# Kernel tuning notes

Hardware: AMD Instinct MI355X
Metric: run time of the kernel (lower is better)

## Reference

```python
import jax, jax.numpy as jnp
import numpy as np

B, S, D, H = 2, 2048, 1024, 16
HD = D // H
NEG = -10000000000.0

def setup_inputs() -> dict:
    key = jax.random.key(0)
    ks = jax.random.split(key, 9)
    s = 1.0 / np.sqrt(D)
    return {
        "x": jax.random.normal(ks[0], (B, S, D), dtype=jnp.float32),
        "Wq": jax.random.uniform(ks[1], (D, D), jnp.float32, -s, s),
        "bq": jax.random.uniform(ks[2], (D,), jnp.float32, -s, s),
        "Wk": jax.random.uniform(ks[3], (D, D), jnp.float32, -s, s),
        "bk": jax.random.uniform(ks[4], (D,), jnp.float32, -s, s),
        "Wv": jax.random.uniform(ks[5], (D, D), jnp.float32, -s, s),
        "bv": jax.random.uniform(ks[6], (D,), jnp.float32, -s, s),
        "Wo": jax.random.uniform(ks[7], (D, D), jnp.float32, -s, s),
        "bo": jax.random.uniform(ks[8], (D,), jnp.float32, -s, s),
    }

def reference(x, Wq, bq, Wk, bk, Wv, bv, Wo, bo):
    b, s, _ = x.shape
    def split_heads(t):
        return t.reshape(b, s, H, HD).transpose(0, 2, 1, 3)  # [b,h,s,hd]
    Q = split_heads(x @ Wq + bq)
    K = split_heads(x @ Wk + bk)
    V = split_heads(x @ Wv + bv)
    scores = jnp.einsum('bhqd,bhkd->bhqk', Q, K) / jnp.sqrt(jnp.float32(HD))
    causal = jnp.tril(jnp.ones((s, s), dtype=bool))
    scores = jnp.where(causal[None, None], scores, NEG)
    attn = jax.nn.softmax(scores, axis=-1)
    ctx = jnp.einsum('bhqk,bhkd->bhqd', attn, V)
    ctx = ctx.transpose(0, 2, 1, 3).reshape(b, s, D)
    return ctx @ Wo + bo
```

## Files before the change

### kernel.cpp

```cpp
#include <hip/hip_runtime.h>
#include <hip/hip_bf16.h>

#define BB 2
#define SS 2048
#define DD 1024
#define HH 16
#define HD 64
#define MM (BB*SS)

typedef __attribute__((ext_vector_type(8))) short bf16x8;
typedef __attribute__((ext_vector_type(4))) float f32x4;
typedef __attribute__((ext_vector_type(16))) float f32x16;

#define QSCALE 0.18033688f

static __device__ __forceinline__ unsigned short f2bf(float f) {
    unsigned int u = __builtin_bit_cast(unsigned int, f);
    u += 0x7fffu + ((u >> 16) & 1u);
    return (unsigned short)(u >> 16);
}

static __device__ __forceinline__ void gload16(const unsigned short* g, unsigned short* l) {
    __builtin_amdgcn_global_load_lds(
        (const __attribute__((address_space(1))) unsigned int*)g,
        (__attribute__((address_space(3))) unsigned int*)l, 16, 0, 0);
}

__global__ __launch_bounds__(256) void prep_kernel(const float* __restrict__ x,
                                                   const float* __restrict__ W0,
                                                   const float* __restrict__ W1,
                                                   const float* __restrict__ W2,
                                                   const float* __restrict__ W3,
                                                   unsigned short* __restrict__ xb,
                                                   unsigned short* __restrict__ Wt)
{
    const int t = threadIdx.x;
    const int bid = blockIdx.x;
    if (bid < 2048) {
        const size_t i = ((size_t)bid * 256 + t) * 8;
        float4 a = *(const float4*)(x + i);
        float4 b = *(const float4*)(x + i + 4);
        union { unsigned short u[8]; bf16x8 v; } pk;
        pk.u[0] = f2bf(a.x); pk.u[1] = f2bf(a.y); pk.u[2] = f2bf(a.z); pk.u[3] = f2bf(a.w);
        pk.u[4] = f2bf(b.x); pk.u[5] = f2bf(b.y); pk.u[6] = f2bf(b.z); pk.u[7] = f2bf(b.w);
        *(bf16x8*)(xb + i) = pk.v;
        return;
    }
    __shared__ unsigned short Ts[64][72];
    const int wsel = (bid - 2048) >> 8;
    const int rem  = (bid - 2048) & 255;
    const float* W = wsel == 0 ? W0 : wsel == 1 ? W1 : wsel == 2 ? W2 : W3;
    unsigned short* out = Wt + (size_t)wsel * DD * DD;
    const int n0 = (rem & 15) * 64, k0 = (rem >> 4) * 64;
#pragma unroll
    for (int i = 0; i < 4; ++i) {
        const int r = (t >> 4) + i * 16;
        const int c = (t & 15) * 4;
        float4 v = *(const float4*)(W + (size_t)(k0 + r) * DD + n0 + c);
        Ts[c + 0][r] = f2bf(v.x); Ts[c + 1][r] = f2bf(v.y);
        Ts[c + 2][r] = f2bf(v.z); Ts[c + 3][r] = f2bf(v.w);
    }
    __syncthreads();
#pragma unroll
    for (int j = 0; j < 2; ++j) {
        const int ch = j * 256 + t;
        const int rn = ch >> 3, ck = (ch & 7) * 8;
        bf16x8 v = *(const bf16x8*)&Ts[rn][ck];
        *(bf16x8*)(out + (size_t)(n0 + rn) * DD + k0 + ck) = v;
    }
}

__global__ __launch_bounds__(256) void gemm_mfma(const unsigned short* __restrict__ A,
                                                 const unsigned short* __restrict__ Bt,
                                                 const float* __restrict__ bias0,
                                                 const float* __restrict__ bias1,
                                                 const float* __restrict__ bias2,
                                                 unsigned short* __restrict__ Qb,
                                                 unsigned short* __restrict__ Kb,
                                                 unsigned short* __restrict__ Vb,
                                                 float* __restrict__ outf,
                                                 int mode)
{
    __shared__ unsigned short As[2][128 * 64];
    __shared__ unsigned short Bs[2][128 * 64];

    const int t = threadIdx.x;
    const int w = t >> 6, l = t & 63;
    const int lane16 = l & 15, quad = l >> 4;
    const int m0 = blockIdx.x * 128, n0 = blockIdx.y * 128;
    const int wm = (w & 1) * 64, wn = (w >> 1) * 64;

    f32x4 acc[4][4] = {};

    int srow[4], skcg[4];
#pragma unroll
    for (int j = 0; j < 4; ++j) {
        const int c = t + j * 256;
        srow[j] = c >> 3;
        skcg[j] = (c & 7) ^ (srow[j] & 7);
    }

#pragma unroll
    for (int j = 0; j < 4; ++j) {
        const int c = t + j * 256;
        gload16(A  + (size_t)(m0 + srow[j]) * DD + skcg[j] * 8, &As[0][c * 8]);
        gload16(Bt + (size_t)(n0 + srow[j]) * DD + skcg[j] * 8, &Bs[0][c * 8]);
    }
    __syncthreads();

#pragma unroll 2
    for (int kt = 0; kt < 16; ++kt) {
        const int cur = kt & 1;
        if (kt + 1 < 16) {
            const int k1 = (kt + 1) * 64;
#pragma unroll
            for (int j = 0; j < 4; ++j) {
                const int c = t + j * 256;
                gload16(A  + (size_t)(m0 + srow[j]) * DD + k1 + skcg[j] * 8, &As[cur ^ 1][c * 8]);
                gload16(Bt + (size_t)(n0 + srow[j]) * DD + k1 + skcg[j] * 8, &Bs[cur ^ 1][c * 8]);
            }
        }
#pragma unroll
        for (int h = 0; h < 2; ++h) {
            bf16x8 af[4], bfr[4];
#pragma unroll
            for (int mt = 0; mt < 4; ++mt) {
                const int row = wm + mt * 16 + lane16;
                af[mt] = *(const bf16x8*)&As[cur][(row * 8 + ((h * 4 + quad) ^ (row & 7))) * 8];
            }
#pragma unroll
            for (int nt = 0; nt < 4; ++nt) {
                const int row = wn + nt * 16 + lane16;
                bfr[nt] = *(const bf16x8*)&Bs[cur][(row * 8 + ((h * 4 + quad) ^ (row & 7))) * 8];
            }
#pragma unroll
            for (int mt = 0; mt < 4; ++mt)
#pragma unroll
                for (int nt = 0; nt < 4; ++nt)
                    acc[mt][nt] = __builtin_amdgcn_mfma_f32_16x16x32_bf16(af[mt], bfr[nt], acc[mt][nt], 0, 0, 0);
        }
        __syncthreads();
    }

    if (mode == 0) {
        const int which = n0 >> 10;
        const float* bias = which == 0 ? bias0 : which == 1 ? bias1 : bias2;
#pragma unroll
        for (int nt = 0; nt < 4; ++nt) {
            const int gcol = n0 + wn + nt * 16 + lane16;
            const int cd = gcol & 1023;
            const float bv = bias[cd];
            const int h_ = cd >> 6, d = cd & 63;
            if (which == 2) {
#pragma unroll
                for (int mt = 0; mt < 4; ++mt) {
                    const int row0 = m0 + wm + mt * 16 + quad * 4;
                    const int b_ = row0 >> 11, s0 = row0 & 2047;
                    union { unsigned short u[4]; uint2 v; } pk;
#pragma unroll
                    for (int r = 0; r < 4; ++r) pk.u[r] = f2bf(acc[mt][nt][r] + bv);
                    *(uint2*)(Vb + ((size_t)(b_ * HH + h_) * HD + d) * SS + s0) = pk.v;
                }
            } else {
                unsigned short* dst3 = which == 0 ? Qb : Kb;
                const float sc_ = which == 0 ? QSCALE : 1.0f;
#pragma unroll
                for (int mt = 0; mt < 4; ++mt)
#pragma unroll
                    for (int r = 0; r < 4; ++r) {
                        const int row = m0 + wm + mt * 16 + quad * 4 + r;
                        const int b_ = row >> 11, s_ = row & 2047;
                        dst3[(((size_t)(b_ * HH + h_) * SS + s_) * HD) + d] =
                            f2bf((acc[mt][nt][r] + bv) * sc_);
                    }
            }
        }
    } else {
#pragma unroll
        for (int nt = 0; nt < 4; ++nt) {
            const int gcol = n0 + wn + nt * 16 + lane16;
            const float bv = bias0[gcol];
#pragma unroll
            for (int mt = 0; mt < 4; ++mt)
#pragma unroll
                for (int r = 0; r < 4; ++r) {
                    const int row = m0 + wm + mt * 16 + quad * 4 + r;
                    outf[(size_t)row * DD + gcol] = acc[mt][nt][r] + bv;
                }
        }
    }
}

__global__ __launch_bounds__(512) void attn_mfma(const unsigned short* __restrict__ Q,
                                                 const unsigned short* __restrict__ K,
                                                 const unsigned short* __restrict__ V,
                                                 unsigned short* __restrict__ ctx)
{
    __shared__ unsigned short Ks[4][4096];
    __shared__ unsigned short Vs[4][4096];

    const int t = threadIdx.x;
    const int w = t >> 6, l = t & 63;
    const int l31 = l & 31, hi = l >> 5;
    const int qg = w & 3, par = w >> 2;
    const int bid = blockIdx.x;
    const int halfg = bid >> 8, idx = bid & 255;
    const int qb_ = idx >> 5;
    const int qblk = halfg ? qb_ : 15 - qb_;
    const int hb = idx & 31;
    const int h = hb & 15, b = hb >> 4;
    const int q0 = qblk * 128;
    const size_t bh = (size_t)(b * HH + h) * SS;
    const unsigned short* Vg = V + (size_t)(b * HH + h) * HD * SS;

    const int wq0 = q0 + qg * 32;
    bf16x8 qf[4];
#pragma unroll
    for (int dt = 0; dt < 4; ++dt)
        qf[dt] = *(const bf16x8*)(Q + (bh + wq0 + l31) * HD + dt * 16 + hi * 8);

    f32x16 ot[2] = {};
    float lp = 0.f;

    const int ntiles = 2 * qblk + 2;
    const int sr = t >> 3;
    const int sg = (t & 7) ^ (sr & 7);

    {
        gload16(K  + (bh + sr) * HD + sg * 8,            &Ks[0][t * 8]);
        gload16(K  + (bh + 64 + sr) * HD + sg * 8,       &Ks[1][t * 8]);
        gload16(Vg + (size_t)sr * SS + sg * 8,           &Vs[0][t * 8]);
        gload16(Vg + (size_t)sr * SS + 64 + sg * 8,      &Vs[1][t * 8]);
    }
    __syncthreads();

    const int nsup = ntiles >> 1;
    for (int st = 0; st < nsup; ++st) {
        if (2 * st + 2 < ntiles) {
            const int ka = (2 * st + 2) * 64, kb = ka + 64;
            const int ba = (2 * st + 2) & 3, bb2 = (2 * st + 3) & 3;
            gload16(K  + (bh + ka + sr) * HD + sg * 8,       &Ks[ba][t * 8]);
            gload16(K  + (bh + kb + sr) * HD + sg * 8,       &Ks[bb2][t * 8]);
            gload16(Vg + (size_t)sr * SS + ka + sg * 8,      &Vs[ba][t * 8]);
            gload16(Vg + (size_t)sr * SS + kb + sg * 8,      &Vs[bb2][t * 8]);
        }

        const int mt = 2 * st + par;
        const int k0 = mt * 64;
        if (k0 <= wq0 + 31) {
            const unsigned short* Kt = Ks[mt & 3];
            const unsigned short* Vt = Vs[mt & 3];

            f32x16 s[2] = {};
#pragma unroll
            for (int dt = 0; dt < 4; ++dt) {
#pragma unroll
                for (int kh = 0; kh < 2; ++kh) {
                    const int row = kh * 32 + l31;
                    bf16x8 kf = *(const bf16x8*)&Kt[(row * 8 + ((dt * 2 + hi) ^ (row & 7))) * 8];
                    s[kh] = __builtin_amdgcn_mfma_f32_32x32x16_bf16(kf, qf[dt], s[kh], 0, 0, 0);
                }
            }

            if (k0 + 63 > wq0) {
                const int q = wq0 + l31;
#pragma unroll
                for (int kh = 0; kh < 2; ++kh)
#pragma unroll
                    for (int r = 0; r < 16; ++r) {
                        const int k = k0 + kh * 32 + (r & 3) + 8 * (r >> 2) + 4 * hi;
                        if (k > q) s[kh][r] = -1e30f;
                    }
            }

#pragma unroll
            for (int kh = 0; kh < 2; ++kh) {
#pragma unroll
                for (int r = 0; r < 16; ++r) s[kh][r] = __builtin_amdgcn_exp2f(s[kh][r]);
                const float t0 = (s[kh][0] + s[kh][1]) + (s[kh][2] + s[kh][3]);
                const float t1 = (s[kh][4] + s[kh][5]) + (s[kh][6] + s[kh][7]);
                const float t2 = (s[kh][8] + s[kh][9]) + (s[kh][10] + s[kh][11]);
                const float t3 = (s[kh][12] + s[kh][13]) + (s[kh][14] + s[kh][15]);
                lp += (t0 + t1) + (t2 + t3);
            }

#pragma unroll
            for (int kh = 0; kh < 2; ++kh) {
#pragma unroll
                for (int c = 0; c < 2; ++c) {
                    const int rb = c * 8;
                    unsigned int w0, w1, w2, w3;
                    asm("v_cvt_pk_bf16_f32 %0, %1, %2" : "=v"(w0) : "v"(s[kh][rb + 0]), "v"(s[kh][rb + 1]));
                    asm("v_cvt_pk_bf16_f32 %0, %1, %2" : "=v"(w2) : "v"(s[kh][rb + 4]), "v"(s[kh][rb + 5]));
                    asm("v_cvt_pk_bf16_f32 %0, %1, %2" : "=v"(w1) : "v"(s[kh][rb + 2]), "v"(s[kh][rb + 3]));
                    asm("v_cvt_pk_bf16_f32 %0, %1, %2" : "=v"(w3) : "v"(s[kh][rb + 6]), "v"(s[kh][rb + 7]));
                    asm("v_permlane32_swap_b32 %0, %1" : "+v"(w0), "+v"(w2));
                    asm("v_permlane32_swap_b32 %0, %1" : "+v"(w1), "+v"(w3));
                    union { unsigned int u[4]; bf16x8 v; } pa;
                    pa.u[0] = w0; pa.u[1] = w1; pa.u[2] = w2; pa.u[3] = w3;
                    const int chunk = kh * 4 + c * 2 + hi;
                    const int rlo = l31, rhi2 = 32 + l31;
                    bf16x8 v0 = *(const bf16x8*)&Vt[(rlo * 8 + (chunk ^ (rlo & 7))) * 8];
                    bf16x8 v1 = *(const bf16x8*)&Vt[(rhi2 * 8 + (chunk ^ (rhi2 & 7))) * 8];
                    ot[0] = __builtin_amdgcn_mfma_f32_32x32x16_bf16(v0, pa.v, ot[0], 0, 0, 0);
                    ot[1] = __builtin_amdgcn_mfma_f32_32x32x16_bf16(v1, pa.v, ot[1], 0, 0, 0);
                }
            }
        }
        __syncthreads();
    }

    float* Osh = (float*)&Ks[0][0];
    float* Lsh = (float*)&Vs[0][0];
    if (par == 1) {
        float* o = Osh + qg * 2048;
#pragma unroll
        for (int a2 = 0; a2 < 2; ++a2)
#pragma unroll
            for (int r = 0; r < 16; ++r) o[(a2 * 16 + r) * 64 + l] = ot[a2][r];
        Lsh[qg * 64 + l] = lp;
    }
    __syncthreads();
    if (par == 0) {
        float* o = Osh + qg * 2048;
#pragma unroll
        for (int a2 = 0; a2 < 2; ++a2)
#pragma unroll
            for (int r = 0; r < 16; ++r) ot[a2][r] += o[(a2 * 16 + r) * 64 + l];
        lp += Lsh[qg * 64 + l];

        lp += __shfl_xor(lp, 32);
        const float inv = 1.f / lp;

        const int qrow = wq0 + l31;
        unsigned short* dst = ctx + ((size_t)(b * SS) + qrow) * DD + h * HD;
#pragma unroll
        for (int a2 = 0; a2 < 2; ++a2)
#pragma unroll
            for (int u = 0; u < 4; ++u) {
                const int d0 = a2 * 32 + 8 * u + 4 * hi;
                union { unsigned short u4[4]; uint2 v; } pk;
#pragma unroll
                for (int r = 0; r < 4; ++r) pk.u4[r] = f2bf(ot[a2][4 * u + r] * inv);
                *(uint2*)(dst + d0) = pk.v;
            }
    }
}

extern "C" void kernel_launch(void* const* d_in, const int* in_sizes, int n_in,
                              void* d_out, int out_size, void* d_ws, size_t ws_size,
                              hipStream_t stream) {
    const float* x  = (const float*)d_in[0];
    const float* Wq = (const float*)d_in[1];
    const float* bq = (const float*)d_in[2];
    const float* Wk = (const float*)d_in[3];
    const float* bk = (const float*)d_in[4];
    const float* Wv = (const float*)d_in[5];
    const float* bv = (const float*)d_in[6];
    const float* Wo = (const float*)d_in[7];
    const float* bo = (const float*)d_in[8];
    float* out = (float*)d_out;

    unsigned short* xb  = (unsigned short*)d_ws;
    unsigned short* Wt  = xb  + (size_t)MM * DD;
    unsigned short* Qb  = Wt  + (size_t)4 * DD * DD;
    unsigned short* Kb  = Qb  + (size_t)MM * DD;
    unsigned short* Vb  = Kb  + (size_t)MM * DD;
    unsigned short* ctxb = Vb + (size_t)MM * DD;

    prep_kernel<<<2048 + 1024, 256, 0, stream>>>(x, Wq, Wk, Wv, Wo, xb, Wt);

    gemm_mfma<<<dim3(MM / 128, 3072 / 128), 256, 0, stream>>>(
        xb, Wt, bq, bk, bv, Qb, Kb, Vb, nullptr, 0);

    attn_mfma<<<(SS / 128) * HH * BB, 512, 0, stream>>>(Qb, Kb, Vb, ctxb);

    gemm_mfma<<<dim3(MM / 128, DD / 128), 256, 0, stream>>>(
        ctxb, Wt + (size_t)3 * DD * DD, bo, nullptr, nullptr,
        nullptr, nullptr, nullptr, out, 1);
}
```

Baseline: 183.3 us.

## Template GEMM on M tile, halve K step, use 64-row tiles for output projection

```diff
diff --git a/kernel.cpp b/kernel.cpp
--- a/kernel.cpp
+++ b/kernel.cpp
@@ -70,6 +70,7 @@
     }
 }
 
+template<int BM>
 __global__ __launch_bounds__(256) void gemm_mfma(const unsigned short* __restrict__ A,
                                                  const unsigned short* __restrict__ Bt,
                                                  const float* __restrict__ bias0,
@@ -81,64 +82,71 @@
                                                  float* __restrict__ outf,
                                                  int mode)
 {
-    __shared__ unsigned short As[2][128 * 64];
-    __shared__ unsigned short Bs[2][128 * 64];
+    constexpr int MT = BM / 32;
+    constexpr int NA = (BM * 4) / 256;
+
+    __shared__ unsigned short As[2][BM * 32];
+    __shared__ unsigned short Bs[2][128 * 32];
 
     const int t = threadIdx.x;
     const int w = t >> 6, l = t & 63;
     const int lane16 = l & 15, quad = l >> 4;
-    const int m0 = blockIdx.x * 128, n0 = blockIdx.y * 128;
-    const int wm = (w & 1) * 64, wn = (w >> 1) * 64;
-
-    f32x4 acc[4][4] = {};
-
-    int srow[4], skcg[4];
-#pragma unroll
-    for (int j = 0; j < 4; ++j) {
+    const int m0 = blockIdx.x * BM, n0 = blockIdx.y * 128;
+    const int wm = (w & 1) * (BM / 2), wn = (w >> 1) * 64;
+
+    f32x4 acc[MT][4] = {};
+
+    int arow[NA], agc[NA];
+#pragma unroll
+    for (int j = 0; j < NA; ++j) {
         const int c = t + j * 256;
-        srow[j] = c >> 3;
-        skcg[j] = (c & 7) ^ (srow[j] & 7);
-    }
-
-#pragma unroll
-    for (int j = 0; j < 4; ++j) {
+        arow[j] = c >> 2;
+        agc[j] = (c & 3) ^ ((arow[j] >> 1) & 3);
+    }
+    int brow[2], bgc[2];
+#pragma unroll
+    for (int j = 0; j < 2; ++j) {
         const int c = t + j * 256;
-        gload16(A  + (size_t)(m0 + srow[j]) * DD + skcg[j] * 8, &As[0][c * 8]);
-        gload16(Bt + (size_t)(n0 + srow[j]) * DD + skcg[j] * 8, &Bs[0][c * 8]);
-    }
+        brow[j] = c >> 2;
+        bgc[j] = (c & 3) ^ ((brow[j] >> 1) & 3);
+    }
+
+#pragma unroll
+    for (int j = 0; j < NA; ++j)
+        gload16(A + (size_t)(m0 + arow[j]) * DD + agc[j] * 8, &As[0][(t + j * 256) * 8]);
+#pragma unroll
+    for (int j = 0; j < 2; ++j)
+        gload16(Bt + (size_t)(n0 + brow[j]) * DD + bgc[j] * 8, &Bs[0][(t + j * 256) * 8]);
     __syncthreads();
 
 #pragma unroll 2
-    for (int kt = 0; kt < 16; ++kt) {
+    for (int kt = 0; kt < 32; ++kt) {
         const int cur = kt & 1;
-        if (kt + 1 < 16) {
-            const int k1 = (kt + 1) * 64;
-#pragma unroll
-            for (int j = 0; j < 4; ++j) {
-                const int c = t + j * 256;
-                gload16(A  + (size_t)(m0 + srow[j]) * DD + k1 + skcg[j] * 8, &As[cur ^ 1][c * 8]);
-                gload16(Bt + (size_t)(n0 + srow[j]) * DD + k1 + skcg[j] * 8, &Bs[cur ^ 1][c * 8]);
-            }
-        }
-#pragma unroll
-        for (int h = 0; h < 2; ++h) {
-            bf16x8 af[4], bfr[4];
-#pragma unroll
-            for (int mt = 0; mt < 4; ++mt) {
-                const int row = wm + mt * 16 + lane16;
-                af[mt] = *(const bf16x8*)&As[cur][(row * 8 + ((h * 4 + quad) ^ (row & 7))) * 8];
-            }
-#pragma unroll
-            for (int nt = 0; nt < 4; ++nt) {
-                const int row = wn + nt * 16 + lane16;
-                bfr[nt] = *(const bf16x8*)&Bs[cur][(row * 8 + ((h * 4 + quad) ^ (row & 7))) * 8];
-            }
-#pragma unroll
-            for (int mt = 0; mt < 4; ++mt)
-#pragma unroll
-                for (int nt = 0; nt < 4; ++nt)
-                    acc[mt][nt] = __builtin_amdgcn_mfma_f32_16x16x32_bf16(af[mt], bfr[nt], acc[mt][nt], 0, 0, 0);
-        }
+        if (kt + 1 < 32) {
+            const int k1 = (kt + 1) * 32;
+#pragma unroll
+            for (int j = 0; j < NA; ++j)
+                gload16(A + (size_t)(m0 + arow[j]) * DD + k1 + agc[j] * 8, &As[cur ^ 1][(t + j * 256) * 8]);
+#pragma unroll
+            for (int j = 0; j < 2; ++j)
+                gload16(Bt + (size_t)(n0 + brow[j]) * DD + k1 + bgc[j] * 8, &Bs[cur ^ 1][(t + j * 256) * 8]);
+        }
+        bf16x8 af[MT], bfr[4];
+#pragma unroll
+        for (int mt = 0; mt < MT; ++mt) {
+            const int row = wm + mt * 16 + lane16;
+            af[mt] = *(const bf16x8*)&As[cur][(row * 4 + (quad ^ ((row >> 1) & 3))) * 8];
+        }
+#pragma unroll
+        for (int nt = 0; nt < 4; ++nt) {
+            const int row = wn + nt * 16 + lane16;
+            bfr[nt] = *(const bf16x8*)&Bs[cur][(row * 4 + (quad ^ ((row >> 1) & 3))) * 8];
+        }
+#pragma unroll
+        for (int mt = 0; mt < MT; ++mt)
+#pragma unroll
+            for (int nt = 0; nt < 4; ++nt)
+                acc[mt][nt] = __builtin_amdgcn_mfma_f32_16x16x32_bf16(af[mt], bfr[nt], acc[mt][nt], 0, 0, 0);
         __syncthreads();
     }
 
@@ -153,7 +161,7 @@
             const int h_ = cd >> 6, d = cd & 63;
             if (which == 2) {
 #pragma unroll
-                for (int mt = 0; mt < 4; ++mt) {
+                for (int mt = 0; mt < MT; ++mt) {
                     const int row0 = m0 + wm + mt * 16 + quad * 4;
                     const int b_ = row0 >> 11, s0 = row0 & 2047;
                     union { unsigned short u[4]; uint2 v; } pk;
@@ -165,7 +173,7 @@
                 unsigned short* dst3 = which == 0 ? Qb : Kb;
                 const float sc_ = which == 0 ? QSCALE : 1.0f;
 #pragma unroll
-                for (int mt = 0; mt < 4; ++mt)
+                for (int mt = 0; mt < MT; ++mt)
 #pragma unroll
                     for (int r = 0; r < 4; ++r) {
                         const int row = m0 + wm + mt * 16 + quad * 4 + r;
@@ -181,7 +189,7 @@
             const int gcol = n0 + wn + nt * 16 + lane16;
             const float bv = bias0[gcol];
 #pragma unroll
-            for (int mt = 0; mt < 4; ++mt)
+            for (int mt = 0; mt < MT; ++mt)
 #pragma unroll
                 for (int r = 0; r < 4; ++r) {
                     const int row = m0 + wm + mt * 16 + quad * 4 + r;
@@ -370,12 +378,12 @@
 
     prep_kernel<<<2048 + 1024, 256, 0, stream>>>(x, Wq, Wk, Wv, Wo, xb, Wt);
 
-    gemm_mfma<<<dim3(MM / 128, 3072 / 128), 256, 0, stream>>>(
+    gemm_mfma<128><<<dim3(MM / 128, 3072 / 128), 256, 0, stream>>>(
         xb, Wt, bq, bk, bv, Qb, Kb, Vb, nullptr, 0);
 
     attn_mfma<<<(SS / 128) * HH * BB, 512, 0, stream>>>(Qb, Kb, Vb, ctxb);
 
-    gemm_mfma<<<dim3(MM / 128, DD / 128), 256, 0, stream>>>(
+    gemm_mfma<64><<<dim3(MM / 64, DD / 128), 256, 0, stream>>>(
         ctxb, Wt + (size_t)3 * DD * DD, bo, nullptr, nullptr,
         nullptr, nullptr, nullptr, out, 1);
 }
```

New measurement: 194.5 us. 1.06x slower.
